# Kernel tuning notes

Hardware: AMD Instinct MI355X
Metric: run time of the kernel (lower is better)

Reference implementation:

```python
import jax, jax.numpy as jnp
import numpy as np

B, T, C, H = 8, 2048, 1024, 64

def setup_inputs() -> dict:
    key = jax.random.key(0)
    k0, k1, k2, k3 = jax.random.split(key, 4)
    s = C ** -0.5
    return {
        "x": jax.random.normal(k0, (B, T, C), dtype=jnp.float32),
        "Wq": jax.random.normal(k1, (C, H), dtype=jnp.float32) * s,
        "Wk": jax.random.normal(k2, (C, H), dtype=jnp.float32) * s,
        "Wv": jax.random.normal(k3, (C, H), dtype=jnp.float32) * s,
    }

def reference(x, Wq, Wk, Wv):
    # x: [B,T,C]; Wq/Wk/Wv: [C,H]
    q = jnp.einsum('btc,ch->bth', x, Wq)
    k = jnp.einsum('btc,ch->bth', x, Wk)
    v = jnp.einsum('btc,ch->bth', x, Wv)
    Tn, Cn = x.shape[1], x.shape[2]
    # NOTE: original scales by C**-0.5 (n_embed), not head_size**-0.5
    wei = jnp.einsum('bqh,bkh->bqk', q, k) * (Cn ** -0.5)  # [B,T,T]
    causal = jnp.tril(jnp.ones((Tn, Tn), dtype=bool))
    wei = jnp.where(causal, wei, -jnp.inf)
    wei = jax.nn.softmax(wei, axis=-1)
    # dropout is identity in eval mode
    out = jnp.einsum('bqk,bkh->bqh', wei, v)  # [B,T,H]
    return out
```

## Files before the change

### kernel.cpp

```cpp
#include <hip/hip_runtime.h>
#include <hip/hip_bf16.h>

typedef __attribute__((ext_vector_type(8))) short short8;
typedef __attribute__((ext_vector_type(4))) float f32x4;
typedef __attribute__((ext_vector_type(4))) unsigned short u16x4;
typedef unsigned short u16;

#define Bn 8
#define Tn 2048
#define Cn 1024
#define Hn 64
#define Mrows (Bn * Tn)

__device__ __forceinline__ u16 bfu(float f) {
    __hip_bfloat16 h = __float2bfloat16(f);
    union { __hip_bfloat16 h; u16 u; } c; c.h = h; return c.u;
}

__device__ __forceinline__ short8 cvt8(f32x4 a0, f32x4 a1) {
    short8 r;
    r[0] = (short)bfu(a0[0]); r[1] = (short)bfu(a0[1]);
    r[2] = (short)bfu(a0[2]); r[3] = (short)bfu(a0[3]);
    r[4] = (short)bfu(a1[0]); r[5] = (short)bfu(a1[1]);
    r[6] = (short)bfu(a1[2]); r[7] = (short)bfu(a1[3]);
    return r;
}

__global__ void convert_w3(const float* __restrict__ Wq, const float* __restrict__ Wk,
                           const float* __restrict__ Wv, u16* __restrict__ wtf, float qscale) {
    int widx = blockIdx.x * 256 + threadIdx.x;
    int mat = widx >> 16;
    int rem = widx & 65535;
    int k = rem >> 6, n = rem & 63;
    const float* W = mat == 0 ? Wq : (mat == 1 ? Wk : Wv);
    float s = mat == 0 ? qscale : 1.0f;
    int ct = mat * 4 + (n >> 4);
    int lane = ((k >> 3) & 3) * 16 + (n & 15);
    wtf[(size_t)(ct * 32 + (k >> 5)) * 512 + lane * 8 + (k & 7)] = bfu(W[rem] * s);
}

__global__ __launch_bounds__(256, 8) void qkv_proj(const float* __restrict__ x,
                                                   const u16* __restrict__ wtf,
                                                   u16* __restrict__ qfl,
                                                   u16* __restrict__ kfl,
                                                   u16* __restrict__ vfl) {
    __shared__ u16 As[2][16][136];
    const int tid = threadIdx.x;
    const int lane = tid & 63;
    const int wn = tid >> 6;
    const int l15 = lane & 15;
    const int lhi = lane >> 4;
    const int row0 = blockIdx.x * 16;

    const int arow = tid >> 4;
    const int ac0 = (tid & 15) * 8;
    const float* asrc = x + (size_t)(row0 + arow) * Cn + ac0;

    f32x4 acc[3];
    for (int nj = 0; nj < 3; ++nj) acc[nj] = f32x4{0.f, 0.f, 0.f, 0.f};

    f32x4 r0 = *(const f32x4*)(asrc);
    f32x4 r1 = *(const f32x4*)(asrc + 4);
    *(short8*)&As[0][arow][ac0] = cvt8(r0, r1);
    r0 = *(const f32x4*)(asrc + 128);
    r1 = *(const f32x4*)(asrc + 132);
    __syncthreads();

    for (int ks = 0; ks < 8; ++ks) {
        const int cur = ks & 1;
        if (ks < 7) {
            *(short8*)&As[cur ^ 1][arow][ac0] = cvt8(r0, r1);
            if (ks < 6) {
                const float* nsrc = asrc + (size_t)(ks + 2) * 128;
                r0 = *(const f32x4*)(nsrc);
                r1 = *(const f32x4*)(nsrc + 4);
            }
        }
        #pragma unroll
        for (int kc = 0; kc < 4; ++kc) {
            short8 af = *(const short8*)&As[cur][l15][kc * 32 + lhi * 8];
            #pragma unroll
            for (int nj = 0; nj < 3; ++nj) {
                short8 bf = *(const short8*)(wtf + (size_t)((wn * 3 + nj) * 32 + ks * 4 + kc) * 512 + lane * 8);
                acc[nj] = __builtin_amdgcn_mfma_f32_16x16x32_bf16(af, bf, acc[nj], 0, 0, 0);
            }
        }
        __syncthreads();
    }

    const int growb = row0 + lhi * 4;
    const int bI = growb >> 11;
    const int tloc = growb & 2047;
    #pragma unroll
    for (int nj = 0; nj < 3; ++nj) {
        const int gcolb = wn * 48 + nj * 16;
        const int matid = gcolb >> 6;
        const int d0 = gcolb & 63;
        if (matid < 2) {
            u16* dst = matid == 0 ? qfl : kfl;
            const int g = tloc >> 4;
            const int lhid = ((d0 & 31) + l15) >> 3;
            const size_t base = ((size_t)(bI * 128 + g) * 2 + (d0 >> 5)) * 512
                                + (size_t)lhid * 128 + (l15 & 7);
            for (int r = 0; r < 4; ++r)
                dst[base + (size_t)(lhi * 4 + r) * 8] = bfu(acc[nj][r]);
        } else {
            const int kt64 = tloc >> 6;
            const int tin = tloc & 63;
            const int kcv = tin >> 5;
            const int lhiv = (tin & 31) >> 3;
            const int e0 = tin & 7;
            const int dt = d0 >> 4;
            u16x4 pk;
            pk[0] = bfu(acc[nj][0]); pk[1] = bfu(acc[nj][1]);
            pk[2] = bfu(acc[nj][2]); pk[3] = bfu(acc[nj][3]);
            *(u16x4*)(vfl + ((size_t)((bI * 32 + kt64) * 4 + dt) * 2 + kcv) * 512
                          + (size_t)(lhiv * 16 + l15) * 8 + e0) = pk;
        }
    }
}

__global__ __launch_bounds__(512, 4) void attn_fwd(const u16* __restrict__ qfl,
                                                   const u16* __restrict__ kfl,
                                                   const u16* __restrict__ vfl,
                                                   float* __restrict__ out) {
    __shared__ float o_lds[8][16][68];
    __shared__ float ml_lds[8][2][16];
    __shared__ u16 pl[8][16][72];
    const int tid = threadIdx.x;
    const int lane = tid & 63;
    const int w = tid >> 6;
    const int l15 = lane & 15, lhi = lane >> 4;
    const int idx = (int)blockIdx.x;
    const int qt = 127 - (idx >> 3);
    const int b = idx & 7;
    const int nkt = (qt >> 2) + 1;
    const int q0 = qt * 16;

    const u16* qb = qfl + (size_t)b * 131072;
    const u16* kb = kfl + (size_t)b * 131072;
    const u16* vb = vfl + (size_t)b * 131072;

    short8 qf[2];
    #pragma unroll
    for (int kc = 0; kc < 2; ++kc)
        qf[kc] = *(const short8*)(qb + ((size_t)(qt * 2 + kc) * 64 + lane) * 8);

    float m = -1e30f, lpart = 0.f;
    f32x4 o[4];
    for (int dt = 0; dt < 4; ++dt) o[dt] = f32x4{0.f, 0.f, 0.f, 0.f};

    for (int kbi = w; kbi < nkt; kbi += 8) {
        const int k0 = kbi * 64;
        short8 kf[2][4], vf[4][2];
        #pragma unroll
        for (int kc = 0; kc < 2; ++kc)
            #pragma unroll
            for (int kt = 0; kt < 4; ++kt)
                kf[kc][kt] = *(const short8*)(kb + ((size_t)((kbi * 4 + kt) * 2 + kc) * 64 + lane) * 8);
        #pragma unroll
        for (int dt = 0; dt < 4; ++dt)
            #pragma unroll
            for (int kc = 0; kc < 2; ++kc)
                vf[dt][kc] = *(const short8*)(vb + ((size_t)((kbi * 4 + dt) * 2 + kc) * 512 + lane * 8));

        f32x4 sacc[4];
        for (int kt = 0; kt < 4; ++kt) sacc[kt] = f32x4{0.f, 0.f, 0.f, 0.f};
        #pragma unroll
        for (int kc = 0; kc < 2; ++kc)
            #pragma unroll
            for (int kt = 0; kt < 4; ++kt)
                sacc[kt] = __builtin_amdgcn_mfma_f32_16x16x32_bf16(kf[kc][kt], qf[kc], sacc[kt], 0, 0, 0);

        if (kbi == nkt - 1) {
            for (int kt = 0; kt < 4; ++kt)
                for (int r = 0; r < 4; ++r) {
                    int kg = k0 + kt * 16 + lhi * 4 + r;
                    if (kg > q0 + l15) sacc[kt][r] = -3.0e38f;
                }
        }
        f32x4 mx0, mx1;
        for (int e = 0; e < 4; ++e) {
            mx0[e] = fmaxf(sacc[0][e], sacc[1][e]);
            mx1[e] = fmaxf(sacc[2][e], sacc[3][e]);
        }
        float tmax = -3.0e38f;
        for (int e = 0; e < 4; ++e) tmax = fmaxf(tmax, fmaxf(mx0[e], mx1[e]));
        tmax = fmaxf(tmax, __shfl_xor(tmax, 16));
        tmax = fmaxf(tmax, __shfl_xor(tmax, 32));
        if (!__all(tmax <= m + 8.0f)) {
            float mnew = fmaxf(m, tmax);
            float corr = exp2f(m - mnew);
            m = mnew;
            lpart *= corr;
            for (int r = 0; r < 4; ++r) {
                float cr = __shfl(corr, lhi * 4 + r);
                for (int dt = 0; dt < 4; ++dt) o[dt][r] *= cr;
            }
        }
        float psum = 0.f;
        for (int kt = 0; kt < 4; ++kt)
            for (int r = 0; r < 4; ++r) {
                float p = exp2f(sacc[kt][r] - m);
                sacc[kt][r] = p;
                psum += p;
            }
        lpart += psum;
        for (int kt = 0; kt < 4; ++kt) {
            u16x4 pk;
            pk[0] = bfu(sacc[kt][0]); pk[1] = bfu(sacc[kt][1]);
            pk[2] = bfu(sacc[kt][2]); pk[3] = bfu(sacc[kt][3]);
            *(u16x4*)&pl[w][l15][kt * 16 + lhi * 4] = pk;
        }
        short8 pf[2];
        #pragma unroll
        for (int kc = 0; kc < 2; ++kc)
            pf[kc] = *(const short8*)&pl[w][l15][kc * 32 + lhi * 8];
        #pragma unroll
        for (int dt = 0; dt < 4; ++dt)
            #pragma unroll
            for (int kc = 0; kc < 2; ++kc)
                o[dt] = __builtin_amdgcn_mfma_f32_16x16x32_bf16(pf[kc], vf[dt][kc], o[dt], 0, 0, 0);
    }
    float lsum = lpart;
    lsum += __shfl_xor(lsum, 16);
    lsum += __shfl_xor(lsum, 32);

    for (int dt = 0; dt < 4; ++dt)
        for (int r = 0; r < 4; ++r)
            o_lds[w][lhi * 4 + r][dt * 16 + l15] = o[dt][r];
    if (lhi == 0) {
        ml_lds[w][0][l15] = m;
        ml_lds[w][1][l15] = lsum;
    }
    __syncthreads();

    float* ob = out + ((size_t)b * Tn + q0) * Hn;
    #pragma unroll
    for (int i = 0; i < 2; ++i) {
        const int e = tid + 512 * i;
        const int row = e >> 6, d = e & 63;
        float M = -3.0e38f;
        #pragma unroll
        for (int ww = 0; ww < 8; ++ww) M = fmaxf(M, ml_lds[ww][0][row]);
        float L = 0.f, acc = 0.f;
        #pragma unroll
        for (int ww = 0; ww < 8; ++ww) {
            float wgt = exp2f(ml_lds[ww][0][row] - M);
            L += ml_lds[ww][1][row] * wgt;
            acc += o_lds[ww][row][d] * wgt;
        }
        ob[(size_t)row * Hn + d] = acc / L;
    }
}

extern "C" void kernel_launch(void* const* d_in, const int* in_sizes, int n_in,
                              void* d_out, int out_size, void* d_ws, size_t ws_size,
                              hipStream_t stream) {
    const float* x = (const float*)d_in[0];
    const float* Wq = (const float*)d_in[1];
    const float* Wk = (const float*)d_in[2];
    const float* Wv = (const float*)d_in[3];
    float* out = (float*)d_out;
    char* ws = (char*)d_ws;

    u16* wtf = (u16*)ws;
    u16* qfl = (u16*)(ws + 196608 * 2);
    u16* kfl = qfl + (size_t)Bn * 131072;
    u16* vfl = kfl + (size_t)Bn * 131072;

    const float qscale = 0.04508422002778011f;
    convert_w3<<<768, 256, 0, stream>>>(Wq, Wk, Wv, wtf, qscale);
    qkv_proj<<<Mrows / 16, 256, 0, stream>>>(x, wtf, qfl, kfl, vfl);
    attn_fwd<<<1024, 512, 0, stream>>>(qfl, kfl, vfl, out);
}
```

Before: 48.96 us.

## Split QKV projection into single-wave blocks per matrix with LDS-staged epilogue

Restructures the projection so each 64-thread block computes one of Q, K or V for a 16-row tile, with 3072 blocks instead of 1024 four-wave blocks. It drops double buffering and barriers, and stages the Q/K outputs through LDS so they are written as coalesced 16-byte vector stores. In exchange, each x tile is loaded and converted to bf16 three times, which raises global traffic on a memory-bound step and removes overlap between loads and MFMA.

```diff
diff --git a/kernel.cpp b/kernel.cpp
--- a/kernel.cpp
+++ b/kernel.cpp
@@ -39,82 +39,76 @@
     wtf[(size_t)(ct * 32 + (k >> 5)) * 512 + lane * 8 + (k & 7)] = bfu(W[rem] * s);
 }
 
-__global__ __launch_bounds__(256, 8) void qkv_proj(const float* __restrict__ x,
-                                                   const u16* __restrict__ wtf,
-                                                   u16* __restrict__ qfl,
-                                                   u16* __restrict__ kfl,
-                                                   u16* __restrict__ vfl) {
-    __shared__ u16 As[2][16][136];
-    const int tid = threadIdx.x;
-    const int lane = tid & 63;
-    const int wn = tid >> 6;
-    const int l15 = lane & 15;
-    const int lhi = lane >> 4;
-    const int row0 = blockIdx.x * 16;
-
-    const int arow = tid >> 4;
-    const int ac0 = (tid & 15) * 8;
-    const float* asrc = x + (size_t)(row0 + arow) * Cn + ac0;
-
-    f32x4 acc[3];
-    for (int nj = 0; nj < 3; ++nj) acc[nj] = f32x4{0.f, 0.f, 0.f, 0.f};
-
-    f32x4 r0 = *(const f32x4*)(asrc);
-    f32x4 r1 = *(const f32x4*)(asrc + 4);
-    *(short8*)&As[0][arow][ac0] = cvt8(r0, r1);
-    r0 = *(const f32x4*)(asrc + 128);
-    r1 = *(const f32x4*)(asrc + 132);
-    __syncthreads();
-
+__global__ __launch_bounds__(64) void qkv_proj(const float* __restrict__ x,
+                                               const u16* __restrict__ wtf,
+                                               u16* __restrict__ qfl,
+                                               u16* __restrict__ kfl,
+                                               u16* __restrict__ vfl) {
+    __shared__ u16 As[16][136];
+    __shared__ u16 ep[16][68];
+    const int lane = threadIdx.x;
+    const int l15 = lane & 15, lhi = lane >> 4;
+    const int bid = (int)blockIdx.x;
+    const int tile = bid / 3;
+    const int mat = bid - tile * 3;
+    const int row0 = tile * 16;
+
+    const int srow = lane >> 4;
+    const int scol = (lane & 15) * 8;
+
+    f32x4 acc[4];
+    #pragma unroll
+    for (int nj = 0; nj < 4; ++nj) acc[nj] = f32x4{0.f, 0.f, 0.f, 0.f};
+
+    #pragma unroll
     for (int ks = 0; ks < 8; ++ks) {
-        const int cur = ks & 1;
-        if (ks < 7) {
-            *(short8*)&As[cur ^ 1][arow][ac0] = cvt8(r0, r1);
-            if (ks < 6) {
-                const float* nsrc = asrc + (size_t)(ks + 2) * 128;
-                r0 = *(const f32x4*)(nsrc);
-                r1 = *(const f32x4*)(nsrc + 4);
-            }
+        #pragma unroll
+        for (int i = 0; i < 4; ++i) {
+            const float* src = x + (size_t)(row0 + i * 4 + srow) * Cn + ks * 128 + scol;
+            f32x4 a = *(const f32x4*)src;
+            f32x4 b = *(const f32x4*)(src + 4);
+            *(short8*)&As[i * 4 + srow][scol] = cvt8(a, b);
         }
         #pragma unroll
         for (int kc = 0; kc < 4; ++kc) {
-            short8 af = *(const short8*)&As[cur][l15][kc * 32 + lhi * 8];
-            #pragma unroll
-            for (int nj = 0; nj < 3; ++nj) {
-                short8 bf = *(const short8*)(wtf + (size_t)((wn * 3 + nj) * 32 + ks * 4 + kc) * 512 + lane * 8);
+            short8 af = *(const short8*)&As[l15][kc * 32 + lhi * 8];
+            #pragma unroll
+            for (int nj = 0; nj < 4; ++nj) {
+                short8 bf = *(const short8*)(wtf + (size_t)((mat * 4 + nj) * 32 + ks * 4 + kc) * 512 + lane * 8);
                 acc[nj] = __builtin_amdgcn_mfma_f32_16x16x32_bf16(af, bf, acc[nj], 0, 0, 0);
             }
         }
-        __syncthreads();
-    }
-
-    const int growb = row0 + lhi * 4;
-    const int bI = growb >> 11;
-    const int tloc = growb & 2047;
-    #pragma unroll
-    for (int nj = 0; nj < 3; ++nj) {
-        const int gcolb = wn * 48 + nj * 16;
-        const int matid = gcolb >> 6;
-        const int d0 = gcolb & 63;
-        if (matid < 2) {
-            u16* dst = matid == 0 ? qfl : kfl;
-            const int g = tloc >> 4;
-            const int lhid = ((d0 & 31) + l15) >> 3;
-            const size_t base = ((size_t)(bI * 128 + g) * 2 + (d0 >> 5)) * 512
-                                + (size_t)lhid * 128 + (l15 & 7);
+    }
+
+    const int bI = row0 >> 11;
+    const int tloc = row0 & 2047;
+    if (mat < 2) {
+        #pragma unroll
+        for (int nj = 0; nj < 4; ++nj)
+            #pragma unroll
             for (int r = 0; r < 4; ++r)
-                dst[base + (size_t)(lhi * 4 + r) * 8] = bfu(acc[nj][r]);
-        } else {
-            const int kt64 = tloc >> 6;
-            const int tin = tloc & 63;
-            const int kcv = tin >> 5;
-            const int lhiv = (tin & 31) >> 3;
-            const int e0 = tin & 7;
-            const int dt = d0 >> 4;
+                ep[lhi * 4 + r][nj * 16 + l15] = bfu(acc[nj][r]);
+        u16* dst = (mat == 0 ? qfl : kfl) + (size_t)bI * 131072;
+        const int g = tloc >> 4;
+        const int trow = lane & 15, lhid = lane >> 4;
+        #pragma unroll
+        for (int kcf = 0; kcf < 2; ++kcf) {
+            short8 v8 = *(const short8*)&ep[trow][kcf * 32 + lhid * 8];
+            *(short8*)(dst + ((size_t)(g * 2 + kcf)) * 512 + lane * 8) = v8;
+        }
+    } else {
+        const int growb = tloc + lhi * 4;
+        const int kt64 = growb >> 6;
+        const int tin = growb & 63;
+        const int kcv = tin >> 5;
+        const int lhiv = (tin & 31) >> 3;
+        const int e0 = tin & 7;
+        #pragma unroll
+        for (int nj = 0; nj < 4; ++nj) {
             u16x4 pk;
             pk[0] = bfu(acc[nj][0]); pk[1] = bfu(acc[nj][1]);
             pk[2] = bfu(acc[nj][2]); pk[3] = bfu(acc[nj][3]);
-            *(u16x4*)(vfl + ((size_t)((bI * 32 + kt64) * 4 + dt) * 2 + kcv) * 512
+            *(u16x4*)(vfl + ((size_t)((bI * 32 + kt64) * 4 + nj) * 2 + kcv) * 512
                           + (size_t)(lhiv * 16 + l15) * 8 + e0) = pk;
         }
     }
@@ -271,6 +265,6 @@
 
     const float qscale = 0.04508422002778011f;
     convert_w3<<<768, 256, 0, stream>>>(Wq, Wk, Wv, wtf, qscale);
-    qkv_proj<<<Mrows / 16, 256, 0, stream>>>(x, wtf, qfl, kfl, vfl);
+    qkv_proj<<<3072, 64, 0, stream>>>(x, wtf, qfl, kfl, vfl);
     attn_fwd<<<1024, 512, 0, stream>>>(qfl, kfl, vfl, out);
 }
```

Result: slower. 62.84 us (+28.4%).
